# Kernel tuning notes

Hardware: AMD Instinct MI355X
Metric: run time of the kernel (lower is better)

Reference implementation:

```python
import jax, jax.numpy as jnp
import numpy as np
import itertools

F = 3          # num_sparse_features
C = 256        # num_categories
D = 64         # embedding_dim
H = 1024       # hidden_units
ND = 13        # num_dense_features
B = 16384      # batch
COMBOS = [c for r in range(2, F + 1) for c in itertools.combinations(range(F), r)]
WIDE_DIM = C * F + sum(C ** len(c) for c in COMBOS) + ND
DEEP_IN = F * D + ND


def setup_inputs() -> dict:
    key = jax.random.key(0)
    ks = jax.random.split(key, 12)
    sparse_inputs = jax.random.randint(ks[0], (B, F), 0, C, dtype=jnp.int32)
    dense_inputs = jax.random.normal(ks[1], (B, ND), dtype=jnp.float32)
    wide_w = jax.random.normal(ks[2], (WIDE_DIM,), dtype=jnp.float32) * 0.01
    wide_b = jax.random.normal(ks[3], (1,), dtype=jnp.float32) * 0.01
    emb = jax.random.normal(ks[4], (F, C, D), dtype=jnp.float32) * 0.05
    W1 = jax.random.normal(ks[5], (H, DEEP_IN), dtype=jnp.float32) / np.sqrt(DEEP_IN).astype(np.float32)
    b1 = jnp.zeros((H,), jnp.float32)
    W2 = jax.random.normal(ks[6], (H, H), dtype=jnp.float32) / np.sqrt(H).astype(np.float32)
    b2 = jnp.zeros((H,), jnp.float32)
    W3 = jax.random.normal(ks[7], (1, H), dtype=jnp.float32) / np.sqrt(H).astype(np.float32)
    b3 = jnp.zeros((1,), jnp.float32)
    return {"sparse_inputs": sparse_inputs, "dense_inputs": dense_inputs,
            "wide_w": wide_w, "wide_b": wide_b, "emb": emb,
            "W1": W1, "b1": b1, "W2": W2, "b2": b2, "W3": W3, "b3": b3}


def reference(sparse_inputs, dense_inputs, wide_w, wide_b, emb, W1, b1, W2, b2, W3, b3):
    # Wide path: one_hot(x) @ W.T  ==  gather of W columns at the hot indices.
    wide = wide_b[0]  # scalar, broadcasts to [B]
    for i in range(F):  # per-feature one-hot block, width C each
        wide = wide + wide_w[i * C + sparse_inputs[:, i]]
    off = F * C
    for combo in COMBOS:  # cross-feature one-hot blocks, width C**len(combo)
        cross = sparse_inputs[:, combo[0]]
        for j in combo[1:]:
            # faithful to source: multiplies by num_sparse_features (F), not C
            cross = cross * F + sparse_inputs[:, j]
        wide = wide + wide_w[off + cross]
        off += C ** len(combo)
    wide = wide + dense_inputs @ wide_w[off:off + ND]  # dense tail of wide linear
    wide = wide[:, None]  # [B, 1]

    # Deep path: per-feature embedding lookup -> concat -> 3-layer MLP
    embedded = jnp.concatenate([emb[i][sparse_inputs[:, i]] for i in range(F)], axis=1)  # [B, F*D]
    deep_x = jnp.concatenate([embedded, dense_inputs], axis=1)  # [B, DEEP_IN]
    h = jax.nn.relu(deep_x @ W1.T + b1)
    h = jax.nn.relu(h @ W2.T + b2)
    deep = h @ W3.T + b3  # [B, 1]

    return jax.nn.sigmoid(wide + deep)
```

## Files before the change

kernel.cpp:

```cpp
#include <hip/hip_runtime.h>
#include <stdint.h>


#define BATCH 16384
#define HDIM 1024
#define K1 224
#define DEEP_IN 205

typedef short bf16x8 __attribute__((ext_vector_type(8)));
typedef float f32x4 __attribute__((ext_vector_type(4)));
typedef uint16_t u16x8 __attribute__((ext_vector_type(8)));
typedef uint16_t u16x4 __attribute__((ext_vector_type(4)));

__device__ __forceinline__ uint16_t f2bf(float f) {
    uint32_t x;
    __builtin_memcpy(&x, &f, 4);
    uint32_t r = (x + 0x7fffu + ((x >> 16) & 1u)) >> 16;
    return (uint16_t)r;
}

__device__ __forceinline__ void async_ld16(const uint16_t* g, uint16_t* l) {
    __builtin_amdgcn_global_load_lds(
        (const __attribute__((address_space(1))) uint32_t*)g,
        (__attribute__((address_space(3))) uint32_t*)l, 16, 0, 0);
}

__global__ __launch_bounds__(256) void prep_kernel(
    const int* __restrict__ sp, const float* __restrict__ dense,
    const float* __restrict__ emb, const float* __restrict__ W1,
    uint16_t* __restrict__ dx, uint16_t* __restrict__ W1b)
{
    const int bid = blockIdx.x;
    if (bid < 1792) {
        int idx = bid * 256 + threadIdx.x;
        int b = idx / 28, c0 = (idx - b * 28) * 8;
        u16x8 o;
        if (c0 < 192) {
            int f = c0 >> 6, cc = c0 & 63;
            int s = sp[b * 3 + f];
            const float* e = emb + (size_t)(((f << 8) + s) * 64 + cc);
            float4 v0 = *(const float4*)e;
            float4 v1 = *(const float4*)(e + 4);
            o[0] = f2bf(v0.x); o[1] = f2bf(v0.y); o[2] = f2bf(v0.z); o[3] = f2bf(v0.w);
            o[4] = f2bf(v1.x); o[5] = f2bf(v1.y); o[6] = f2bf(v1.z); o[7] = f2bf(v1.w);
        } else {
#pragma unroll
            for (int t = 0; t < 8; t++) {
                int c = c0 + t;
                o[t] = (c < DEEP_IN) ? f2bf(dense[b * 13 + (c - 192)])
                                     : (uint16_t)0;
            }
        }
        *(u16x8*)(dx + (size_t)b * K1 + c0) = o;
    } else {
        int idx = (bid - 1792) * 256 + threadIdx.x;
        int n = idx / 28, c0 = (idx - n * 28) * 8;
        u16x8 o;
#pragma unroll
        for (int t = 0; t < 8; t++) {
            int c = c0 + t;
            o[t] = (c < DEEP_IN) ? f2bf(W1[n * DEEP_IN + c]) : (uint16_t)0;
        }
        *(u16x8*)(W1b + (size_t)n * K1 + c0) = o;
    }
}

#define GEMM_CORE(A_, B_, K_)                                                  \
    const int lane = tid & 63;                                                 \
    const int wave = tid >> 6;                                                 \
    const int wm = wave >> 2;                                                  \
    const int wn = wave & 3;                                                   \
    const int xcd = id & 7;                                                    \
    const int slot = id >> 3;                                                  \
    const int mbX = (M >> 7) >> 3;                                             \
    const int by = xcd * mbX + (slot >> 2);                                    \
    const int bx = slot & 3;                                                   \
    const int bm = by * 128;                                                   \
    const int bn = bx * 256;                                                   \
    const int rl = lane & 15, q = lane >> 4;                                   \
    f32x4 acc[4][4];                                                           \
    _Pragma("unroll") for (int i = 0; i < 4; i++)                              \
        _Pragma("unroll") for (int j = 0; j < 4; j++) acc[i][j] = (f32x4)0.f;  \
    const int c0 = 2 * wave, c1 = 2 * wave + 1;                                \
    const uint16_t* aS = A_ + (size_t)(bm + wave * 16 + rl) * K_ + q * 8;      \
    const uint16_t* bS0 = B_ + (size_t)(bn + (c0 >> 2) * 64 + 4 * rl + (c0 & 3)) * K_ + q * 8; \
    const uint16_t* bS1 = B_ + (size_t)(bn + (c1 >> 2) * 64 + 4 * rl + (c1 & 3)) * K_ + q * 8; \
    const int dA = wave * 512, dB0 = c0 * 512, dB1 = c1 * 512;                 \
    async_ld16(aS, &Al[0][dA]);                                                \
    async_ld16(bS0, &Bl[0][dB0]);                                              \
    async_ld16(bS1, &Bl[0][dB1]);                                              \
    asm volatile("s_waitcnt vmcnt(0)" ::: "memory");                           \
    __syncthreads();                                                           \
    int p = 0;                                                                 \
    for (int k0 = 32; k0 < K_; k0 += 32) {                                     \
        async_ld16(aS + k0, &Al[p ^ 1][dA]);                                   \
        async_ld16(bS0 + k0, &Bl[p ^ 1][dB0]);                                 \
        async_ld16(bS1 + k0, &Bl[p ^ 1][dB1]);                                 \
        bf16x8 af[4], bfr[4];                                                  \
        _Pragma("unroll") for (int i = 0; i < 4; i++)                          \
            af[i] = *(const bf16x8*)&Al[p][(wm * 4 + i) * 512 + lane * 8];     \
        _Pragma("unroll") for (int j = 0; j < 4; j++)                          \
            bfr[j] = *(const bf16x8*)&Bl[p][(wn * 4 + j) * 512 + lane * 8];    \
        _Pragma("unroll") for (int i = 0; i < 4; i++)                          \
            _Pragma("unroll") for (int j = 0; j < 4; j++)                      \
                acc[i][j] = __builtin_amdgcn_mfma_f32_16x16x32_bf16(           \
                    af[i], bfr[j], acc[i][j], 0, 0, 0);                        \
        asm volatile("s_waitcnt vmcnt(0)" ::: "memory");                       \
        __syncthreads();                                                       \
        p ^= 1;                                                                \
    }                                                                          \
    {                                                                          \
        bf16x8 af[4], bfr[4];                                                  \
        _Pragma("unroll") for (int i = 0; i < 4; i++)                          \
            af[i] = *(const bf16x8*)&Al[p][(wm * 4 + i) * 512 + lane * 8];     \
        _Pragma("unroll") for (int j = 0; j < 4; j++)                          \
            bfr[j] = *(const bf16x8*)&Bl[p][(wn * 4 + j) * 512 + lane * 8];    \
        _Pragma("unroll") for (int i = 0; i < 4; i++)                          \
            _Pragma("unroll") for (int j = 0; j < 4; j++)                      \
                acc[i][j] = __builtin_amdgcn_mfma_f32_16x16x32_bf16(           \
                    af[i], bfr[j], acc[i][j], 0, 0, 0);                        \
    }

__global__ __launch_bounds__(512, 4) void gemm_relu(
    const uint16_t* __restrict__ A, const uint16_t* __restrict__ Bw,
    const float* __restrict__ bias, uint16_t* __restrict__ C,
    const float* __restrict__ W2, uint16_t* __restrict__ W2b,
    const int* __restrict__ sp, const float* __restrict__ dense,
    const float* __restrict__ ww, const float* __restrict__ wb,
    const float* __restrict__ b3, float* __restrict__ wide,
    int M, int N, int K)
{
    const int id = blockIdx.x;
    const int tid = threadIdx.x;

    if (id >= 512) {
        if (id < 768) {
            int k = (id - 512) * 512 + tid;
            const float* src = W2 + (size_t)k * 8;
            float4 v0 = *(const float4*)src;
            float4 v1 = *(const float4*)(src + 4);
            u16x8 o;
            o[0] = f2bf(v0.x); o[1] = f2bf(v0.y); o[2] = f2bf(v0.z); o[3] = f2bf(v0.w);
            o[4] = f2bf(v1.x); o[5] = f2bf(v1.y); o[6] = f2bf(v1.z); o[7] = f2bf(v1.w);
            *(u16x8*)(W2b + (size_t)k * 8) = o;
        } else {
            int b = (id - 768) * 512 + tid;
            int s0 = sp[b * 3], s1 = sp[b * 3 + 1], s2 = sp[b * 3 + 2];
            float w = wb[0] + b3[0];
            w += ww[s0] + ww[256 + s1] + ww[512 + s2];
            w += ww[768    + s0 * 3 + s1];
            w += ww[66304  + s0 * 3 + s2];
            w += ww[131840 + s1 * 3 + s2];
            w += ww[197376 + (s0 * 3 + s1) * 3 + s2];
            const float* wd = ww + 16974592;
            float acc2 = 0.f;
#pragma unroll
            for (int j = 0; j < 13; j++) acc2 += dense[b * 13 + j] * wd[j];
            wide[b] = w + acc2;
        }
        return;
    }

    __shared__ __align__(16) uint16_t Al[2][4096];
    __shared__ __align__(16) uint16_t Bl[2][8192];
    GEMM_CORE(A, Bw, K)

    float bv[4];
#pragma unroll
    for (int j = 0; j < 4; j++) bv[j] = bias[bn + wn * 64 + 4 * rl + j];
#pragma unroll
    for (int i = 0; i < 4; i++) {
#pragma unroll
        for (int r = 0; r < 4; r++) {
            int m = bm + wm * 64 + i * 16 + q * 4 + r;
            u16x4 o;
#pragma unroll
            for (int j = 0; j < 4; j++)
                o[j] = f2bf(fmaxf(acc[i][j][r] + bv[j], 0.f));
            *(u16x4*)&C[(size_t)m * N + bn + wn * 64 + 4 * rl] = o;
        }
    }
}

__global__ __launch_bounds__(512, 4) void gemm_fused(
    const uint16_t* __restrict__ A, const uint16_t* __restrict__ Bw,
    const float* __restrict__ bias, const float* __restrict__ W3,
    float* __restrict__ outacc, int M, int N, int K)
{
    const int id = blockIdx.x;
    const int tid = threadIdx.x;
    __shared__ __align__(16) uint16_t Al[2][4096];
    __shared__ __align__(16) uint16_t Bl[2][8192];
    GEMM_CORE(A, Bw, K)

    float bv[4], w3v[4];
#pragma unroll
    for (int j = 0; j < 4; j++) {
        int n = bn + wn * 64 + 4 * rl + j;
        bv[j] = bias[n];
        w3v[j] = W3[n];
    }
#pragma unroll
    for (int i = 0; i < 4; i++) {
#pragma unroll
        for (int r = 0; r < 4; r++) {
            float pt = 0.f;
#pragma unroll
            for (int j = 0; j < 4; j++)
                pt += fmaxf(acc[i][j][r] + bv[j], 0.f) * w3v[j];
            pt += __shfl_xor(pt, 1);
            pt += __shfl_xor(pt, 2);
            pt += __shfl_xor(pt, 4);
            pt += __shfl_xor(pt, 8);
            if (rl == 0) {
                int m = bm + wm * 64 + i * 16 + q * 4 + r;
                atomicAdd(&outacc[m], pt);
            }
        }
    }
}

__global__ __launch_bounds__(256) void sigmoid_kernel(
    const float* __restrict__ outacc, float* __restrict__ out)
{
    int b = blockIdx.x * 256 + threadIdx.x;
    out[b] = 1.f / (1.f + __expf(-outacc[b]));
}

extern "C" void kernel_launch(void* const* d_in, const int* in_sizes, int n_in,
                              void* d_out, int out_size, void* d_ws, size_t ws_size,
                              hipStream_t stream) {
    const int*   sp    = (const int*)d_in[0];
    const float* dense = (const float*)d_in[1];
    const float* ww    = (const float*)d_in[2];
    const float* wb    = (const float*)d_in[3];
    const float* emb   = (const float*)d_in[4];
    const float* W1    = (const float*)d_in[5];
    const float* b1    = (const float*)d_in[6];
    const float* W2    = (const float*)d_in[7];
    const float* b2    = (const float*)d_in[8];
    const float* W3    = (const float*)d_in[9];
    const float* b3    = (const float*)d_in[10];
    float* out = (float*)d_out;

    char* ws = (char*)d_ws;
    float*    wide = (float*)ws;
    uint16_t* dxp  = (uint16_t*)(ws + 65536);
    uint16_t* W1b  = (uint16_t*)(ws + 7405568);
    uint16_t* W2b  = (uint16_t*)(ws + 7864320);
    uint16_t* h1   = (uint16_t*)(ws + 9961472);

    prep_kernel<<<1904, 256, 0, stream>>>(sp, dense, emb, W1, dxp, W1b);
    gemm_relu<<<800, 512, 0, stream>>>(
        dxp, W1b, b1, h1, W2, W2b, sp, dense, ww, wb, b3, wide,
        BATCH, HDIM, K1);
    gemm_fused<<<(BATCH / 128) * 4, 512, 0, stream>>>(
        h1, W2b, b2, W3, wide, BATCH, HDIM, HDIM);
    sigmoid_kernel<<<BATCH / 256, 256, 0, stream>>>(wide, out);
}
```

Measured before the change: 181.9 us.

## Fuse all stages into one cooperative persistent kernel with grid syncs

Replaces the four separate launches (prep, first GEMM, second GEMM with W3 reduction, sigmoid) with one cooperative kernel of 256 blocks that runs every stage and separates them with grid-wide barriers. Each block handles two GEMM tiles per layer, and the conversion, wide-path and sigmoid work run as grid-stride loops inside the same kernel. The aim is to remove kernel launch gaps and tail effects between stages. In exchange it runs only 256 blocks of 512 threads, which can lower occupancy and latency hiding compared with the 512-block GEMM launches, and each grid.sync adds its own cost. If the cooperative launch fails, the old four-kernel path runs instead.

```diff
diff --git a/kernel.cpp b/kernel.cpp
--- a/kernel.cpp
+++ b/kernel.cpp
@@ -1,4 +1,5 @@
 #include <hip/hip_runtime.h>
+#include <hip/hip_cooperative_groups.h>
 #include <stdint.h>
 
 
@@ -25,53 +26,13 @@
         (__attribute__((address_space(3))) uint32_t*)l, 16, 0, 0);
 }
 
-__global__ __launch_bounds__(256) void prep_kernel(
-    const int* __restrict__ sp, const float* __restrict__ dense,
-    const float* __restrict__ emb, const float* __restrict__ W1,
-    uint16_t* __restrict__ dx, uint16_t* __restrict__ W1b)
-{
-    const int bid = blockIdx.x;
-    if (bid < 1792) {
-        int idx = bid * 256 + threadIdx.x;
-        int b = idx / 28, c0 = (idx - b * 28) * 8;
-        u16x8 o;
-        if (c0 < 192) {
-            int f = c0 >> 6, cc = c0 & 63;
-            int s = sp[b * 3 + f];
-            const float* e = emb + (size_t)(((f << 8) + s) * 64 + cc);
-            float4 v0 = *(const float4*)e;
-            float4 v1 = *(const float4*)(e + 4);
-            o[0] = f2bf(v0.x); o[1] = f2bf(v0.y); o[2] = f2bf(v0.z); o[3] = f2bf(v0.w);
-            o[4] = f2bf(v1.x); o[5] = f2bf(v1.y); o[6] = f2bf(v1.z); o[7] = f2bf(v1.w);
-        } else {
-#pragma unroll
-            for (int t = 0; t < 8; t++) {
-                int c = c0 + t;
-                o[t] = (c < DEEP_IN) ? f2bf(dense[b * 13 + (c - 192)])
-                                     : (uint16_t)0;
-            }
-        }
-        *(u16x8*)(dx + (size_t)b * K1 + c0) = o;
-    } else {
-        int idx = (bid - 1792) * 256 + threadIdx.x;
-        int n = idx / 28, c0 = (idx - n * 28) * 8;
-        u16x8 o;
-#pragma unroll
-        for (int t = 0; t < 8; t++) {
-            int c = c0 + t;
-            o[t] = (c < DEEP_IN) ? f2bf(W1[n * DEEP_IN + c]) : (uint16_t)0;
-        }
-        *(u16x8*)(W1b + (size_t)n * K1 + c0) = o;
-    }
-}
-
-#define GEMM_CORE(A_, B_, K_)                                                  \
+#define GEMM_CORE(A_, B_, K_, ID_)                                             \
     const int lane = tid & 63;                                                 \
     const int wave = tid >> 6;                                                 \
     const int wm = wave >> 2;                                                  \
     const int wn = wave & 3;                                                   \
-    const int xcd = id & 7;                                                    \
-    const int slot = id >> 3;                                                  \
+    const int xcd = (ID_) & 7;                                                 \
+    const int slot = (ID_) >> 3;                                               \
     const int mbX = (M >> 7) >> 3;                                             \
     const int by = xcd * mbX + (slot >> 2);                                    \
     const int bx = slot & 3;                                                   \
@@ -81,11 +42,11 @@
     f32x4 acc[4][4];                                                           \
     _Pragma("unroll") for (int i = 0; i < 4; i++)                              \
         _Pragma("unroll") for (int j = 0; j < 4; j++) acc[i][j] = (f32x4)0.f;  \
-    const int c0 = 2 * wave, c1 = 2 * wave + 1;                                \
+    const int cc0 = 2 * wave, cc1 = 2 * wave + 1;                              \
     const uint16_t* aS = A_ + (size_t)(bm + wave * 16 + rl) * K_ + q * 8;      \
-    const uint16_t* bS0 = B_ + (size_t)(bn + (c0 >> 2) * 64 + 4 * rl + (c0 & 3)) * K_ + q * 8; \
-    const uint16_t* bS1 = B_ + (size_t)(bn + (c1 >> 2) * 64 + 4 * rl + (c1 & 3)) * K_ + q * 8; \
-    const int dA = wave * 512, dB0 = c0 * 512, dB1 = c1 * 512;                 \
+    const uint16_t* bS0 = B_ + (size_t)(bn + (cc0 >> 2) * 64 + 4 * rl + (cc0 & 3)) * K_ + q * 8; \
+    const uint16_t* bS1 = B_ + (size_t)(bn + (cc1 >> 2) * 64 + 4 * rl + (cc1 & 3)) * K_ + q * 8; \
+    const int dA = wave * 512, dB0 = cc0 * 512, dB1 = cc1 * 512;               \
     async_ld16(aS, &Al[0][dA]);                                                \
     async_ld16(bS0, &Bl[0][dB0]);                                              \
     async_ld16(bS1, &Bl[0][dB1]);                                              \
@@ -121,6 +82,186 @@
                     af[i], bfr[j], acc[i][j], 0, 0, 0);                        \
     }
 
+__global__ __launch_bounds__(512, 4) void wad_mega(
+    const int* __restrict__ sp, const float* __restrict__ dense,
+    const float* __restrict__ emb, const float* __restrict__ W1,
+    const float* __restrict__ b1, const float* __restrict__ W2,
+    const float* __restrict__ b2, const float* __restrict__ W3,
+    const float* __restrict__ ww, const float* __restrict__ wb,
+    const float* __restrict__ b3,
+    uint16_t* __restrict__ dxp, uint16_t* __restrict__ W1b,
+    uint16_t* __restrict__ W2b, uint16_t* __restrict__ h1,
+    float* __restrict__ wide, float* __restrict__ out)
+{
+    namespace cg = cooperative_groups;
+    cg::grid_group grid = cg::this_grid();
+
+    __shared__ __align__(16) uint16_t Al[2][4096];
+    __shared__ __align__(16) uint16_t Bl[2][8192];
+
+    const int id = blockIdx.x;
+    const int tid = threadIdx.x;
+    const int gt = id * 512 + tid;
+
+    for (int idx = gt; idx < 458752; idx += 131072) {
+        int b = idx / 28, c0 = (idx - b * 28) * 8;
+        u16x8 o;
+        if (c0 < 192) {
+            int f = c0 >> 6, cc = c0 & 63;
+            int s = sp[b * 3 + f];
+            const float* e = emb + (size_t)(((f << 8) + s) * 64 + cc);
+            float4 v0 = *(const float4*)e;
+            float4 v1 = *(const float4*)(e + 4);
+            o[0] = f2bf(v0.x); o[1] = f2bf(v0.y); o[2] = f2bf(v0.z); o[3] = f2bf(v0.w);
+            o[4] = f2bf(v1.x); o[5] = f2bf(v1.y); o[6] = f2bf(v1.z); o[7] = f2bf(v1.w);
+        } else {
+#pragma unroll
+            for (int t = 0; t < 8; t++) {
+                int c = c0 + t;
+                o[t] = (c < DEEP_IN) ? f2bf(dense[b * 13 + (c - 192)])
+                                     : (uint16_t)0;
+            }
+        }
+        *(u16x8*)(dxp + (size_t)b * K1 + c0) = o;
+    }
+    if (gt < 28672) {
+        int n = gt / 28, c0 = (gt - n * 28) * 8;
+        u16x8 o;
+#pragma unroll
+        for (int t = 0; t < 8; t++) {
+            int c = c0 + t;
+            o[t] = (c < DEEP_IN) ? f2bf(W1[n * DEEP_IN + c]) : (uint16_t)0;
+        }
+        *(u16x8*)(W1b + (size_t)n * K1 + c0) = o;
+    }
+    {
+        const float* src = W2 + (size_t)gt * 8;
+        float4 v0 = *(const float4*)src;
+        float4 v1 = *(const float4*)(src + 4);
+        u16x8 o;
+        o[0] = f2bf(v0.x); o[1] = f2bf(v0.y); o[2] = f2bf(v0.z); o[3] = f2bf(v0.w);
+        o[4] = f2bf(v1.x); o[5] = f2bf(v1.y); o[6] = f2bf(v1.z); o[7] = f2bf(v1.w);
+        *(u16x8*)(W2b + (size_t)gt * 8) = o;
+    }
+    if (gt < BATCH) {
+        int b = gt;
+        int s0 = sp[b * 3], s1 = sp[b * 3 + 1], s2 = sp[b * 3 + 2];
+        float w = wb[0] + b3[0];
+        w += ww[s0] + ww[256 + s1] + ww[512 + s2];
+        w += ww[768    + s0 * 3 + s1];
+        w += ww[66304  + s0 * 3 + s2];
+        w += ww[131840 + s1 * 3 + s2];
+        w += ww[197376 + (s0 * 3 + s1) * 3 + s2];
+        const float* wd = ww + 16974592;
+        float a2 = 0.f;
+#pragma unroll
+        for (int j = 0; j < 13; j++) a2 += dense[b * 13 + j] * wd[j];
+        wide[b] = w + a2;
+    }
+
+    grid.sync();
+
+#pragma unroll 1
+    for (int t = 0; t < 2; ++t) {
+        __syncthreads();
+        const int M = BATCH;
+        GEMM_CORE(dxp, W1b, K1, id + t * 256)
+        float bv[4];
+#pragma unroll
+        for (int j = 0; j < 4; j++) bv[j] = b1[bn + wn * 64 + 4 * rl + j];
+#pragma unroll
+        for (int i = 0; i < 4; i++) {
+#pragma unroll
+            for (int r = 0; r < 4; r++) {
+                int m = bm + wm * 64 + i * 16 + q * 4 + r;
+                u16x4 o;
+#pragma unroll
+                for (int j = 0; j < 4; j++)
+                    o[j] = f2bf(fmaxf(acc[i][j][r] + bv[j], 0.f));
+                *(u16x4*)&h1[(size_t)m * HDIM + bn + wn * 64 + 4 * rl] = o;
+            }
+        }
+    }
+
+    grid.sync();
+
+#pragma unroll 1
+    for (int t = 0; t < 2; ++t) {
+        __syncthreads();
+        const int M = BATCH;
+        GEMM_CORE(h1, W2b, HDIM, id + t * 256)
+        float bv[4], w3v[4];
+#pragma unroll
+        for (int j = 0; j < 4; j++) {
+            int n = bn + wn * 64 + 4 * rl + j;
+            bv[j] = b2[n];
+            w3v[j] = W3[n];
+        }
+#pragma unroll
+        for (int i = 0; i < 4; i++) {
+#pragma unroll
+            for (int r = 0; r < 4; r++) {
+                float pt = 0.f;
+#pragma unroll
+                for (int j = 0; j < 4; j++)
+                    pt += fmaxf(acc[i][j][r] + bv[j], 0.f) * w3v[j];
+                pt += __shfl_xor(pt, 1);
+                pt += __shfl_xor(pt, 2);
+                pt += __shfl_xor(pt, 4);
+                pt += __shfl_xor(pt, 8);
+                if (rl == 0) {
+                    int m = bm + wm * 64 + i * 16 + q * 4 + r;
+                    atomicAdd(&wide[m], pt);
+                }
+            }
+        }
+    }
+
+    grid.sync();
+
+    if (gt < BATCH) out[gt] = 1.f / (1.f + __expf(-wide[gt]));
+}
+
+__global__ __launch_bounds__(256) void prep_kernel(
+    const int* __restrict__ sp, const float* __restrict__ dense,
+    const float* __restrict__ emb, const float* __restrict__ W1,
+    uint16_t* __restrict__ dx, uint16_t* __restrict__ W1b)
+{
+    const int bid = blockIdx.x;
+    if (bid < 1792) {
+        int idx = bid * 256 + threadIdx.x;
+        int b = idx / 28, c0 = (idx - b * 28) * 8;
+        u16x8 o;
+        if (c0 < 192) {
+            int f = c0 >> 6, cc = c0 & 63;
+            int s = sp[b * 3 + f];
+            const float* e = emb + (size_t)(((f << 8) + s) * 64 + cc);
+            float4 v0 = *(const float4*)e;
+            float4 v1 = *(const float4*)(e + 4);
+            o[0] = f2bf(v0.x); o[1] = f2bf(v0.y); o[2] = f2bf(v0.z); o[3] = f2bf(v0.w);
+            o[4] = f2bf(v1.x); o[5] = f2bf(v1.y); o[6] = f2bf(v1.z); o[7] = f2bf(v1.w);
+        } else {
+#pragma unroll
+            for (int t = 0; t < 8; t++) {
+                int c = c0 + t;
+                o[t] = (c < DEEP_IN) ? f2bf(dense[b * 13 + (c - 192)])
+                                     : (uint16_t)0;
+            }
+        }
+        *(u16x8*)(dx + (size_t)b * K1 + c0) = o;
+    } else {
+        int idx = (bid - 1792) * 256 + threadIdx.x;
+        int n = idx / 28, c0 = (idx - n * 28) * 8;
+        u16x8 o;
+#pragma unroll
+        for (int t = 0; t < 8; t++) {
+            int c = c0 + t;
+            o[t] = (c < DEEP_IN) ? f2bf(W1[n * DEEP_IN + c]) : (uint16_t)0;
+        }
+        *(u16x8*)(W1b + (size_t)n * K1 + c0) = o;
+    }
+}
+
 __global__ __launch_bounds__(512, 4) void gemm_relu(
     const uint16_t* __restrict__ A, const uint16_t* __restrict__ Bw,
     const float* __restrict__ bias, uint16_t* __restrict__ C,
@@ -163,8 +304,7 @@
 
     __shared__ __align__(16) uint16_t Al[2][4096];
     __shared__ __align__(16) uint16_t Bl[2][8192];
-    GEMM_CORE(A, Bw, K)
-
+    GEMM_CORE(A, Bw, K, id)
     float bv[4];
 #pragma unroll
     for (int j = 0; j < 4; j++) bv[j] = bias[bn + wn * 64 + 4 * rl + j];
@@ -191,8 +331,7 @@
     const int tid = threadIdx.x;
     __shared__ __align__(16) uint16_t Al[2][4096];
     __shared__ __align__(16) uint16_t Bl[2][8192];
-    GEMM_CORE(A, Bw, K)
-
+    GEMM_CORE(A, Bw, K, id)
     float bv[4], w3v[4];
 #pragma unroll
     for (int j = 0; j < 4; j++) {
@@ -250,11 +389,22 @@
     uint16_t* W2b  = (uint16_t*)(ws + 7864320);
     uint16_t* h1   = (uint16_t*)(ws + 9961472);
 
-    prep_kernel<<<1904, 256, 0, stream>>>(sp, dense, emb, W1, dxp, W1b);
-    gemm_relu<<<800, 512, 0, stream>>>(
-        dxp, W1b, b1, h1, W2, W2b, sp, dense, ww, wb, b3, wide,
-        BATCH, HDIM, K1);
-    gemm_fused<<<(BATCH / 128) * 4, 512, 0, stream>>>(
-        h1, W2b, b2, W3, wide, BATCH, HDIM, HDIM);
-    sigmoid_kernel<<<BATCH / 256, 256, 0, stream>>>(wide, out);
-}
+    void* args[] = {
+        (void*)&sp, (void*)&dense, (void*)&emb, (void*)&W1, (void*)&b1,
+        (void*)&W2, (void*)&b2, (void*)&W3, (void*)&ww, (void*)&wb,
+        (void*)&b3, (void*)&dxp, (void*)&W1b, (void*)&W2b, (void*)&h1,
+        (void*)&wide, (void*)&out
+    };
+    hipError_t err = hipLaunchCooperativeKernel(
+        (const void*)wad_mega, dim3(256), dim3(512), args, 0, stream);
+
+    if (err != hipSuccess) {
+        prep_kernel<<<1904, 256, 0, stream>>>(sp, dense, emb, W1, dxp, W1b);
+        gemm_relu<<<800, 512, 0, stream>>>(
+            dxp, W1b, b1, h1, W2, W2b, sp, dense, ww, wb, b3, wide,
+            BATCH, HDIM, K1);
+        gemm_fused<<<(BATCH / 128) * 4, 512, 0, stream>>>(
+            h1, W2b, b2, W3, wide, BATCH, HDIM, HDIM);
+        sigmoid_kernel<<<BATCH / 256, 256, 0, stream>>>(wide, out);
+    }
+}
```

Measured after the change: 349.1 us. 91.9% more time.
